# Kernel optimization log

Measured on AMD Instinct MI355X. Metric: run time of the kernel, lower is better.

The kernel has to match this reference:

```python
import jax, jax.numpy as jnp
import numpy as np

N = 100000
E = 1600000
IN_DIM = 128
HID = 128
C = 10
N_INJ = 20000
T_HET = 0.5          # self.hetero_level (set by set_adaptation_from_data)
HP_MAX = 1.0         # highpass_scale_max
INJ_LAM = 0.8        # self.inject_lambda


def setup_inputs() -> dict:
    key = jax.random.key(0)
    ks = jax.random.split(key, 16)
    glorot = lambda k, i, o: jax.random.normal(k, (i, o), jnp.float32) * (2.0 / (i + o)) ** 0.5
    return {
        "x": jax.random.normal(ks[0], (N, IN_DIM), jnp.float32),
        "edge_index": jax.random.randint(ks[1], (2, E), 0, N, jnp.int64),
        "inject_indices": jax.random.randint(ks[2], (N_INJ,), 0, N, jnp.int64),
        "initial_preds": jax.random.uniform(ks[3], (N, C), jnp.float32),
        "W1": glorot(ks[4], IN_DIM, HID), "b1": jnp.zeros((HID,), jnp.float32),
        "W2": glorot(ks[5], HID, HID),   "b2": jnp.zeros((HID,), jnp.float32),
        "Wl1": glorot(ks[6], IN_DIM, HID),
        "Wl2": glorot(ks[7], HID, HID),
        "Wm1": glorot(ks[8], HID, HID), "bm1": jnp.zeros((HID,), jnp.float32),
        "Wm2": glorot(ks[9], HID, C),   "bm2": jnp.zeros((C,), jnp.float32),
    }


def _gcn_norm(edge_index):
    # add self loops, symmetric D^{-1/2} (A+I) D^{-1/2} normalization (PyG GCNConv default)
    loops = jnp.arange(N, dtype=edge_index.dtype)
    src = jnp.concatenate([edge_index[0], loops])
    dst = jnp.concatenate([edge_index[1], loops])
    deg = jax.ops.segment_sum(jnp.ones_like(dst, jnp.float32), dst, num_segments=N)
    dinv = jnp.where(deg > 0, jax.lax.rsqrt(jnp.maximum(deg, 1.0)), 0.0)
    norm = dinv[src] * dinv[dst]  # [E+N]
    return src, dst, norm


def _gcn_conv(x, W, b, src, dst, norm):
    h = x @ W                                   # [N, H]
    msg = h[src] * norm[:, None]                # gather + scale, [E+N, H]
    return jax.ops.segment_sum(msg, dst, num_segments=N) + b


def reference(x, edge_index, inject_indices, initial_preds,
              W1, b1, W2, b2, Wl1, Wl2, Wm1, bm1, Wm2, bm2):
    src, dst, norm = _gcn_norm(edge_index)
    mix = T_HET * HP_MAX

    low1 = _gcn_conv(x, W1, b1, src, dst, norm)
    high1 = x @ Wl1 - low1
    h = jax.nn.relu(low1 + mix * high1)        # dropout: eval mode (identity)

    low2 = _gcn_conv(h, W2, b2, src, dst, norm)
    high2 = h @ Wl2 - low2
    h2 = low2 + mix * high2

    logits = jax.nn.relu(h2 @ Wm1 + bm1) @ Wm2 + bm2   # [N, C]
    # indexed injection: logits[idx] = logits[idx] + lam * preds[idx]
    logits = logits.at[inject_indices].set(
        logits[inject_indices] + INJ_LAM * initial_preds[inject_indices])
    return jax.nn.log_softmax(logits, axis=1)
```

## Files before the change

kernel.cpp:

```cpp
#include <hip/hip_runtime.h>
#include <hip/hip_bf16.h>
#include <math.h>

typedef __attribute__((ext_vector_type(8))) short short8;
typedef __attribute__((ext_vector_type(4))) float f32x4;
typedef __attribute__((ext_vector_type(2))) float f32x2;

#define INJ_LAM 0.8f
#define BSH 9
#define BWD 512

__device__ inline float bf2f(unsigned short s){
  union{unsigned u; float f;} v; v.u=((unsigned)s)<<16; return v.f;
}
__device__ inline unsigned short f2bf(float f){
  __hip_bfloat16 h=__float2bfloat16(f);
  return *reinterpret_cast<unsigned short*>(&h);
}
__device__ inline unsigned pack2(float lo, float hi){
  return ((unsigned)f2bf(hi)<<16)|(unsigned)f2bf(lo);
}

__global__ void k_prep(const float* __restrict__ W1,const float* __restrict__ Wl1,
                       const float* __restrict__ W2,const float* __restrict__ Wl2,
                       const float* __restrict__ Wm1,const float* __restrict__ Wm2,
                       const float* __restrict__ b1,const float* __restrict__ b2,
                       unsigned short* __restrict__ Wt1, unsigned short* __restrict__ Wt2,
                       unsigned short* __restrict__ Wm1t, unsigned short* __restrict__ Wm2tp,
                       float* __restrict__ bh1, float* __restrict__ bh2,
                       unsigned* __restrict__ flags32, int nf4,
                       unsigned* __restrict__ bhist8, unsigned* __restrict__ zcur8){
  int i=blockIdx.x*blockDim.x+threadIdx.x;
  if(i<256*128){
    int c=i>>7, k=i&127;
    float v1=(c<128)?W1[k*128+c]:Wl1[k*128+(c-128)];
    float v2=(c<128)?W2[k*128+c]:Wl2[k*128+(c-128)];
    Wt1[i]=f2bf(v1); Wt2[i]=f2bf(v2);
    if(c<128) Wm1t[i]=f2bf(Wm1[k*128+c]);
    if(c<16)  Wm2tp[i]=f2bf((c<10)?Wm2[k*10+c]:0.f);
    if(i<128){ bh1[i]=0.5f*b1[i]; bh2[i]=0.5f*b2[i]; }
  }
  if(i<nf4) flags32[i]=0u;
  if(i<2048){ bhist8[i]=0u; zcur8[i]=0u; }
}

__global__ void k_bhist(const int* __restrict__ dst, unsigned* __restrict__ bhist8, int E){
  __shared__ unsigned lh[256];
  int t=threadIdx.x;
  lh[t]=0u; __syncthreads();
  int base=blockIdx.x*2048;
  #pragma unroll
  for(int k=0;k<8;k++){
    int e=base+k*256+t;
    if(e<E) atomicAdd(&lh[dst[e]>>BSH],1u);
  }
  __syncthreads();
  if(lh[t]) atomicAdd(&bhist8[t*8],lh[t]);
}

__launch_bounds__(256)
__global__ void k_bscatter(const int* __restrict__ src, const int* __restrict__ dst,
                           const unsigned* __restrict__ bhist8, unsigned* __restrict__ zcur8,
                           int* __restrict__ psrc, int* __restrict__ pdst, int E, int NBK){
  __shared__ unsigned lh[256];
  __shared__ unsigned gb[256];
  __shared__ unsigned ss[256];
  int t=threadIdx.x;
  lh[t]=0u;
  unsigned v=(t<NBK)?bhist8[t*8]:0u;
  ss[t]=v; __syncthreads();
  for(int off=1;off<256;off<<=1){
    unsigned u=(t>=off)?ss[t-off]:0u; __syncthreads();
    ss[t]+=u; __syncthreads();
  }
  unsigned bb=ss[t]-v;
  int base=blockIdx.x*2048;
  unsigned lr[8]; int bk[8], sv[8], dv_[8];
  #pragma unroll
  for(int k=0;k<8;k++){
    int e=base+k*256+t;
    if(e<E){
      int d=dst[e]; int b=d>>BSH;
      bk[k]=b; dv_[k]=d; sv[k]=src[e];
      lr[k]=atomicAdd(&lh[b],1u);
    } else bk[k]=-1;
  }
  __syncthreads();
  if(lh[t]) gb[t]=bb+atomicAdd(&zcur8[t*8],lh[t]);
  __syncthreads();
  #pragma unroll
  for(int k=0;k<8;k++){
    if(bk[k]>=0){
      unsigned p=gb[bk[k]]+lr[k];
      psrc[p]=sv[k]; pdst[p]=dv_[k];
    }
  }
}

__launch_bounds__(256)
__global__ void k_bucket(const int* __restrict__ psrc, const int* __restrict__ pdst,
                         const unsigned* __restrict__ bhist8, unsigned* __restrict__ rank,
                         unsigned* __restrict__ meta, float* __restrict__ dinv,
                         int* __restrict__ csr,
                         const int* __restrict__ inj, unsigned char* __restrict__ flag,
                         int N, int NI, int NBK){
  __shared__ unsigned lc[BWD];
  __shared__ unsigned lo[BWD];
  __shared__ unsigned ss[256];
  int b=blockIdx.x, t=threadIdx.x;
  for(int i=b*256+t;i<NI;i+=gridDim.x*256) flag[inj[i]]=1;
  unsigned v=(t<NBK)?bhist8[t*8]:0u;
  ss[t]=v; lc[t]=0u; lc[t+256]=0u;
  __syncthreads();
  for(int off=1;off<256;off<<=1){
    unsigned u=(t>=off)?ss[t-off]:0u; __syncthreads();
    ss[t]+=u; __syncthreads();
  }
  unsigned e1=ss[b];
  unsigned e0=e1-bhist8[b*8];
  __syncthreads();
  int lo_node=b<<BSH;
  for(unsigned p=e0+t;p<e1;p+=256){
    int dl=pdst[p]-lo_node;
    rank[p]=atomicAdd(&lc[dl],1u);
  }
  __syncthreads();
  unsigned c0=lc[2*t], c1=lc[2*t+1], ps=c0+c1;
  ss[t]=ps; __syncthreads();
  for(int off=1;off<256;off<<=1){
    unsigned u=(t>=off)?ss[t-off]:0u; __syncthreads();
    ss[t]+=u; __syncthreads();
  }
  unsigned excl=ss[t]-ps;
  lo[2*t]=excl; lo[2*t+1]=excl+c0;
  __syncthreads();
  #pragma unroll
  for(int k=0;k<2;k++){
    int nl=t+k*256; int node=lo_node+nl;
    if(node<N){
      unsigned c=lc[nl];
      meta[node]=(e0+lo[nl])|(c<<21);
      dinv[node]=rsqrtf((float)(c+1u));
    }
  }
  for(unsigned p=e0+t;p<e1;p+=256){
    int dl=pdst[p]-lo_node;
    csr[e0+lo[dl]+rank[p]]=psrc[p];
  }
}

template<bool FP32IN>
__device__ inline void load_afrag(const void* __restrict__ Xv, size_t arow, int l4, short8* a){
  if(FP32IN){
    const float* X=(const float*)Xv + arow*128 + l4*8;
    #pragma unroll
    for(int ks=0;ks<4;ks++){
      float4 f0=*reinterpret_cast<const float4*>(X+ks*32);
      float4 f1=*reinterpret_cast<const float4*>(X+ks*32+4);
      short8 t;
      t[0]=(short)f2bf(f0.x); t[1]=(short)f2bf(f0.y); t[2]=(short)f2bf(f0.z); t[3]=(short)f2bf(f0.w);
      t[4]=(short)f2bf(f1.x); t[5]=(short)f2bf(f1.y); t[6]=(short)f2bf(f1.z); t[7]=(short)f2bf(f1.w);
      a[ks]=t;
    }
  }else{
    const unsigned short* X=(const unsigned short*)Xv + arow*128 + l4*8;
    #pragma unroll
    for(int ks=0;ks<4;ks++)
      a[ks]=*reinterpret_cast<const short8*>(X+ks*32);
  }
}

template<bool FP32IN>
__launch_bounds__(256, 4)
__global__ void k_gemm(const void* __restrict__ Xv, const unsigned short* __restrict__ Wt,
                       const float* __restrict__ dinv,
                       unsigned short* __restrict__ G, unsigned short* __restrict__ XL, int N){
  int wave=threadIdx.x>>6, lane=threadIdx.x&63;
  int l15=lane&15, l4=lane>>4;
  int blk0=blockIdx.x*128;
  if(blk0>=N) return;
  short8 wf[4][4];
  #pragma unroll
  for(int i=0;i<4;i++){
    int col=(wave*4+i)*16+l15;
    #pragma unroll
    for(int ks=0;ks<4;ks++)
      wf[i][ks]=*reinterpret_cast<const short8*>(Wt+(size_t)col*128+ks*32+l4*8);
  }
  int r0=blk0+l15; if(r0>N-1) r0=N-1;
  short8 aC[4], aN[4];
  load_afrag<FP32IN>(Xv,(size_t)r0,l4,aC);
  #pragma unroll 1
  for(int nt=0;nt<8;nt++){
    int node0=blk0+nt*16;
    if(node0>=N) break;
    if(nt<7){
      int rn=node0+16+l15; if(rn>N-1) rn=N-1;
      load_afrag<FP32IN>(Xv,(size_t)rn,l4,aN);
    }
    f32x4 acc[4];
    #pragma unroll
    for(int i=0;i<4;i++) acc[i]=(f32x4){0.f,0.f,0.f,0.f};
    #pragma unroll
    for(int i=0;i<4;i++){
      #pragma unroll
      for(int ks=0;ks<4;ks++)
        acc[i]=__builtin_amdgcn_mfma_f32_16x16x32_bf16(wf[i][ks],aC[ks],acc[i],0,0,0);
    }
    int node=node0+l15;
    if(node<N){
      if(wave<2){
        float dv=dinv[node];
        #pragma unroll
        for(int i=0;i<4;i++){
          f32x4 v=acc[i];
          uint2 p; p.x=pack2(v[0]*dv,v[1]*dv); p.y=pack2(v[2]*dv,v[3]*dv);
          *reinterpret_cast<uint2*>(G+(size_t)node*128+(wave*4+i)*16+l4*4)=p;
        }
      }else{
        #pragma unroll
        for(int i=0;i<4;i++){
          f32x4 v=acc[i];
          uint2 p; p.x=pack2(v[0]*0.5f,v[1]*0.5f); p.y=pack2(v[2]*0.5f,v[3]*0.5f);
          *reinterpret_cast<uint2*>(XL+(size_t)node*128+((wave-2)*4+i)*16+l4*4)=p;
        }
      }
    }
    #pragma unroll
    for(int ks=0;ks<4;ks++) aC[ks]=aN[ks];
  }
}

#define ADDQ(v) do{ \
  unsigned ux=(unsigned)(v).x, uy=(unsigned)(v).y, uz=(unsigned)(v).z, uw=(unsigned)(v).w; \
  accv[0]+=(f32x2){__uint_as_float(ux<<16),__uint_as_float(ux&0xffff0000u)}; \
  accv[1]+=(f32x2){__uint_as_float(uy<<16),__uint_as_float(uy&0xffff0000u)}; \
  accv[2]+=(f32x2){__uint_as_float(uz<<16),__uint_as_float(uz&0xffff0000u)}; \
  accv[3]+=(f32x2){__uint_as_float(uw<<16),__uint_as_float(uw&0xffff0000u)}; \
}while(0)

template<bool RELU>
__device__ __forceinline__ void conv_node(int node, int N,
    const unsigned short* __restrict__ G, const unsigned short* __restrict__ XL,
    const float* __restrict__ bh, const float* __restrict__ dinv,
    const int* __restrict__ csr, const unsigned* __restrict__ meta,
    unsigned short* __restrict__ ldsrow, int lane){
  if(node>=N) return;
  int g=lane>>4, li=lane&15;
  const int4* Gv=(const int4*)G;
  const int4 Z={0,0,0,0};
  f32x2 accv[4];
  #pragma unroll
  for(int i=0;i<4;i++) accv[i]=(f32x2){0.f,0.f};
  if(g==0){
    int4 v=Gv[(size_t)node*16+li];
    ADDQ(v);
  }
  unsigned mt=meta[node];
  unsigned start=mt&0x1FFFFFu, deg=mt>>21;
  unsigned j=(unsigned)g;
  int4 v0=Z,v1=Z,v2=Z,v3=Z;
  if(j<deg)    v0=Gv[(size_t)csr[start+j]*16+li];
  if(j+4<deg)  v1=Gv[(size_t)csr[start+j+4]*16+li];
  if(j+8<deg)  v2=Gv[(size_t)csr[start+j+8]*16+li];
  if(j+12<deg) v3=Gv[(size_t)csr[start+j+12]*16+li];
  j+=16;
  while(j<deg){
    int4 n0=Gv[(size_t)csr[start+j]*16+li];
    int4 n1=(j+4<deg)?Gv[(size_t)csr[start+j+4]*16+li]:Z;
    int4 n2=(j+8<deg)?Gv[(size_t)csr[start+j+8]*16+li]:Z;
    int4 n3=(j+12<deg)?Gv[(size_t)csr[start+j+12]*16+li]:Z;
    ADDQ(v0); ADDQ(v1); ADDQ(v2); ADDQ(v3);
    v0=n0; v1=n1; v2=n2; v3=n3; j+=16;
  }
  ADDQ(v0); ADDQ(v1); ADDQ(v2); ADDQ(v3);
  float acc[8];
  #pragma unroll
  for(int i=0;i<4;i++){ acc[2*i]=accv[i][0]; acc[2*i+1]=accv[i][1]; }
  #pragma unroll
  for(int i=0;i<8;i++){
    acc[i]+=__shfl_xor(acc[i],16,64);
    acc[i]+=__shfl_xor(acc[i],32,64);
  }
  if(g==0){
    float dv2=0.5f*dinv[node];
    float4 b0=*reinterpret_cast<const float4*>(bh+li*8);
    float4 b1=*reinterpret_cast<const float4*>(bh+li*8+4);
    int4 xv=((const int4*)XL)[(size_t)node*16+li];
    float xl[8];
    { unsigned _x=(unsigned)xv.x,_y=(unsigned)xv.y,_z=(unsigned)xv.z,_w=(unsigned)xv.w;
      xl[0]=bf2f((unsigned short)(_x&0xffffu)); xl[1]=bf2f((unsigned short)(_x>>16));
      xl[2]=bf2f((unsigned short)(_y&0xffffu)); xl[3]=bf2f((unsigned short)(_y>>16));
      xl[4]=bf2f((unsigned short)(_z&0xffffu)); xl[5]=bf2f((unsigned short)(_z>>16));
      xl[6]=bf2f((unsigned short)(_w&0xffffu)); xl[7]=bf2f((unsigned short)(_w>>16)); }
    float bb[8]={b0.x,b0.y,b0.z,b0.w,b1.x,b1.y,b1.z,b1.w};
    float r[8];
    #pragma unroll
    for(int i=0;i<8;i++){
      r[i]=dv2*acc[i]+bb[i]+xl[i];
      if(RELU) r[i]=fmaxf(r[i],0.f);
    }
    int4 o;
    o.x=(int)pack2(r[0],r[1]); o.y=(int)pack2(r[2],r[3]);
    o.z=(int)pack2(r[4],r[5]); o.w=(int)pack2(r[6],r[7]);
    *reinterpret_cast<int4*>(ldsrow+li*8)=o;
  }
}

__launch_bounds__(1024)
__global__ void k_convg(const unsigned short* __restrict__ G1, const unsigned short* __restrict__ XL1,
                        const float* __restrict__ bh1, const float* __restrict__ dinv,
                        const int* __restrict__ csr, const unsigned* __restrict__ meta,
                        const unsigned short* __restrict__ Wt2,
                        unsigned short* __restrict__ G2, unsigned short* __restrict__ XL2, int N){
  __shared__ __align__(16) unsigned short ht[16][136];
  int wave=threadIdx.x>>6, lane=threadIdx.x&63;
  int l15=lane&15, l4=lane>>4;
  int blk0=blockIdx.x*16;
  conv_node<true>(blk0+wave, N, G1, XL1, bh1, dinv, csr, meta, &ht[wave][0], lane);
  __syncthreads();
  short8 wfr[4], a[4];
  #pragma unroll
  for(int ks=0;ks<4;ks++){
    wfr[ks]=*reinterpret_cast<const short8*>(Wt2+(size_t)(wave*16+l15)*128+ks*32+l4*8);
    a[ks]=*reinterpret_cast<const short8*>(&ht[l15][ks*32+l4*8]);
  }
  f32x4 acc=(f32x4){0.f,0.f,0.f,0.f};
  #pragma unroll
  for(int ks=0;ks<4;ks++)
    acc=__builtin_amdgcn_mfma_f32_16x16x32_bf16(wfr[ks],a[ks],acc,0,0,0);
  int node=blk0+l15;
  if(node<N){
    if(wave<8){
      float dv=dinv[node];
      uint2 p; p.x=pack2(acc[0]*dv,acc[1]*dv); p.y=pack2(acc[2]*dv,acc[3]*dv);
      *reinterpret_cast<uint2*>(G2+(size_t)node*128+wave*16+l4*4)=p;
    }else{
      uint2 p; p.x=pack2(acc[0]*0.5f,acc[1]*0.5f); p.y=pack2(acc[2]*0.5f,acc[3]*0.5f);
      *reinterpret_cast<uint2*>(XL2+(size_t)node*128+(wave-8)*16+l4*4)=p;
    }
  }
}

__launch_bounds__(1024)
__global__ void k_convm(const unsigned short* __restrict__ G2, const unsigned short* __restrict__ XL2,
                        const float* __restrict__ bh2, const float* __restrict__ dinv,
                        const int* __restrict__ csr, const unsigned* __restrict__ meta,
                        const unsigned short* __restrict__ Wm1t, const unsigned short* __restrict__ Wm2tp,
                        const float* __restrict__ bm1, const float* __restrict__ bm2,
                        const unsigned char* __restrict__ flag, const float* __restrict__ preds,
                        float* __restrict__ out, int N){
  __shared__ __align__(16) unsigned short ht[16][136];
  __shared__ __align__(16) unsigned short zt[16][136];
  int wave=threadIdx.x>>6, lane=threadIdx.x&63;
  int l15=lane&15, l4=lane>>4;
  int blk0=blockIdx.x*16;
  conv_node<false>(blk0+wave, N, G2, XL2, bh2, dinv, csr, meta, &ht[wave][0], lane);
  __syncthreads();
  if(wave<8){
    int ct=wave;
    short8 wfr[4], a[4];
    #pragma unroll
    for(int ks=0;ks<4;ks++){
      wfr[ks]=*reinterpret_cast<const short8*>(Wm1t+(size_t)(ct*16+l15)*128+ks*32+l4*8);
      a[ks]=*reinterpret_cast<const short8*>(&ht[l15][ks*32+l4*8]);
    }
    f32x4 acc=(f32x4){0.f,0.f,0.f,0.f};
    #pragma unroll
    for(int ks=0;ks<4;ks++)
      acc=__builtin_amdgcn_mfma_f32_16x16x32_bf16(wfr[ks],a[ks],acc,0,0,0);
    float4 bm=*reinterpret_cast<const float4*>(bm1+ct*16+l4*4);
    uint2 p;
    p.x=pack2(fmaxf(acc[0]+bm.x,0.f),fmaxf(acc[1]+bm.y,0.f));
    p.y=pack2(fmaxf(acc[2]+bm.z,0.f),fmaxf(acc[3]+bm.w,0.f));
    *reinterpret_cast<uint2*>(&zt[l15][ct*16+l4*4])=p;
  }
  __syncthreads();
  if(wave==0){
    short8 a2[4], w2[4];
    #pragma unroll
    for(int ks=0;ks<4;ks++){
      a2[ks]=*reinterpret_cast<const short8*>(&zt[l15][ks*32+l4*8]);
      w2[ks]=*reinterpret_cast<const short8*>(Wm2tp+(size_t)l15*128+ks*32+l4*8);
    }
    f32x4 acc2=(f32x4){0.f,0.f,0.f,0.f};
    #pragma unroll
    for(int ks=0;ks<4;ks++)
      acc2=__builtin_amdgcn_mfma_f32_16x16x32_bf16(w2[ks],a2[ks],acc2,0,0,0);
    int node=blk0+l15;
    bool have=node<N;
    int c0=l4*4;
    float v[4];
    #pragma unroll
    for(int k=0;k<4;k++){
      int c=c0+k;
      v[k]=(c<10)?(acc2[k]+bm2[c]):-3.0e38f;
    }
    if(have && c0<10 && flag[node]){
      #pragma unroll
      for(int k=0;k<4;k++){
        int c=c0+k;
        if(c<10) v[k]+=INJ_LAM*preds[(size_t)node*10+c];
      }
    }
    float m=fmaxf(fmaxf(v[0],v[1]),fmaxf(v[2],v[3]));
    m=fmaxf(m,__shfl_xor(m,16,64));
    m=fmaxf(m,__shfl_xor(m,32,64));
    float s=0.f;
    #pragma unroll
    for(int k=0;k<4;k++){ int c=c0+k; if(c<10) s+=expf(v[k]-m); }
    s+=__shfl_xor(s,16,64);
    s+=__shfl_xor(s,32,64);
    float lse=m+logf(s);
    if(have && c0<10){
      float2 o01; o01.x=v[0]-lse; o01.y=v[1]-lse;
      *reinterpret_cast<float2*>(out+(size_t)node*10+c0)=o01;
      if(c0+2<10){
        float2 o23; o23.x=v[2]-lse; o23.y=v[3]-lse;
        *reinterpret_cast<float2*>(out+(size_t)node*10+c0+2)=o23;
      }
    }
  }
}

extern "C" void kernel_launch(void* const* d_in, const int* in_sizes, int n_in,
                              void* d_out, int out_size, void* d_ws, size_t ws_size,
                              hipStream_t stream){
  const float* x    =(const float*)d_in[0];
  const int*   ei   =(const int*)  d_in[1];
  const int*   inj  =(const int*)  d_in[2];
  const float* preds=(const float*)d_in[3];
  const float* W1 =(const float*)d_in[4];  const float* b1 =(const float*)d_in[5];
  const float* W2 =(const float*)d_in[6];  const float* b2 =(const float*)d_in[7];
  const float* Wl1=(const float*)d_in[8];  const float* Wl2=(const float*)d_in[9];
  const float* Wm1=(const float*)d_in[10]; const float* bm1=(const float*)d_in[11];
  const float* Wm2=(const float*)d_in[12]; const float* bm2=(const float*)d_in[13];
  float* out=(float*)d_out;

  const int N  = in_sizes[0]/128;
  const int E  = in_sizes[1]/2;
  const int NI = in_sizes[2];
  const int* srcp = ei;
  const int* dstp = ei+E;
  const int NBK = (N+BWD-1)>>BSH;

  char* w=(char*)d_ws;
  auto carve=[&](size_t sz)->char*{ char* p=w; w+=(sz+255)&~(size_t)255; return p; };
  unsigned short* S1 =(unsigned short*)carve((size_t)N*128*2);
  unsigned short* S2 =(unsigned short*)carve((size_t)N*128*2);
  unsigned short* S3 =(unsigned short*)carve((size_t)N*128*2);
  unsigned short* Wt1=(unsigned short*)carve(256*128*2);
  unsigned short* Wt2=(unsigned short*)carve(256*128*2);
  unsigned short* Wm1t=(unsigned short*)carve(128*128*2);
  unsigned short* Wm2tp=(unsigned short*)carve(16*128*2);
  float*    dinv  =(float*)   carve((size_t)N*4);
  unsigned* meta  =(unsigned*)carve((size_t)N*4);
  int*      csr   =(int*)     carve((size_t)E*4);
  unsigned char* flags=(unsigned char*)carve(((size_t)N+3)&~(size_t)3);
  unsigned* bhist8=(unsigned*)carve(256*8*4);
  unsigned* zcur8 =(unsigned*)carve(256*8*4);
  float* bh1=(float*)carve(128*4);
  float* bh2=(float*)carve(128*4);
  (void)ws_size; (void)n_in; (void)out_size;

  int* psrc=(int*)S3;
  int* pdst=psrc+E;
  unsigned* rank=(unsigned*)S1;

  const int T=256;
  const int EB=(E+2047)/2048;
  const int nf4=(N+3)/4;
  int gp=(32768>nf4?32768:nf4); gp=(gp+T-1)/T;
  hipLaunchKernelGGL(k_prep, dim3(gp), dim3(T), 0, stream,
                     W1,Wl1,W2,Wl2,Wm1,Wm2,b1,b2,
                     Wt1,Wt2,Wm1t,Wm2tp,bh1,bh2,
                     (unsigned*)flags, nf4, bhist8, zcur8);
  hipLaunchKernelGGL(k_bhist, dim3(EB), dim3(T), 0, stream, dstp, bhist8, E);
  hipLaunchKernelGGL(k_bscatter, dim3(EB), dim3(T), 0, stream, srcp, dstp, bhist8, zcur8,
                     psrc, pdst, E, NBK);
  hipLaunchKernelGGL(k_bucket, dim3(NBK), dim3(T), 0, stream, psrc, pdst, bhist8, rank,
                     meta, dinv, csr, inj, flags, N, NI, NBK);
  hipLaunchKernelGGL(k_gemm<true>, dim3((N+127)/128), dim3(T), 0, stream,
                     (const void*)x, Wt1, dinv, S1, S2, N);
  hipLaunchKernelGGL(k_convg, dim3((N+15)/16), dim3(1024), 0, stream,
                     S1, S2, bh1, dinv, csr, meta, Wt2, S2, S3, N);
  hipLaunchKernelGGL(k_convm, dim3((N+15)/16), dim3(1024), 0, stream,
                     S2, S3, bh2, dinv, csr, meta, Wm1t, Wm2tp, bm1, bm2,
                     flags, preds, out, N);
}
```

Measured before the change: 373.6 us.

## Process nodes in degree-sorted order in conv kernels to balance block work

Builds a per-node degree histogram during bucketing and adds a counting-sort kernel that produces a degree-ordered node permutation. Both aggregation kernels then take their nodes through this permutation, so the 16 waves sharing a block and its barrier have similar neighbour counts and wait less on the slowest wave. The cost is one extra small kernel, extra atomics, and per-node indirection that scatters the output-row and metadata accesses that were contiguous before.

```diff
diff --git a/kernel.cpp b/kernel.cpp
--- a/kernel.cpp
+++ b/kernel.cpp
@@ -29,7 +29,8 @@
                        unsigned short* __restrict__ Wm1t, unsigned short* __restrict__ Wm2tp,
                        float* __restrict__ bh1, float* __restrict__ bh2,
                        unsigned* __restrict__ flags32, int nf4,
-                       unsigned* __restrict__ bhist8, unsigned* __restrict__ zcur8){
+                       unsigned* __restrict__ bhist8, unsigned* __restrict__ zcur8,
+                       unsigned* __restrict__ dhist8, unsigned* __restrict__ dcur8){
   int i=blockIdx.x*blockDim.x+threadIdx.x;
   if(i<256*128){
     int c=i>>7, k=i&127;
@@ -42,6 +43,7 @@
   }
   if(i<nf4) flags32[i]=0u;
   if(i<2048){ bhist8[i]=0u; zcur8[i]=0u; }
+  if(i<512){ dhist8[i]=0u; dcur8[i]=0u; }
 }
 
 __global__ void k_bhist(const int* __restrict__ dst, unsigned* __restrict__ bhist8, int E){
@@ -103,14 +105,17 @@
                          unsigned* __restrict__ meta, float* __restrict__ dinv,
                          int* __restrict__ csr,
                          const int* __restrict__ inj, unsigned char* __restrict__ flag,
+                         unsigned* __restrict__ dhist8,
                          int N, int NI, int NBK){
   __shared__ unsigned lc[BWD];
   __shared__ unsigned lo[BWD];
   __shared__ unsigned ss[256];
+  __shared__ unsigned dh[64];
   int b=blockIdx.x, t=threadIdx.x;
   for(int i=b*256+t;i<NI;i+=gridDim.x*256) flag[inj[i]]=1;
   unsigned v=(t<NBK)?bhist8[t*8]:0u;
   ss[t]=v; lc[t]=0u; lc[t+256]=0u;
+  if(t<64) dh[t]=0u;
   __syncthreads();
   for(int off=1;off<256;off<<=1){
     unsigned u=(t>=off)?ss[t-off]:0u; __syncthreads();
@@ -141,12 +146,42 @@
       unsigned c=lc[nl];
       meta[node]=(e0+lo[nl])|(c<<21);
       dinv[node]=rsqrtf((float)(c+1u));
+      unsigned bin=c; if(bin>63u) bin=63u;
+      atomicAdd(&dh[bin],1u);
     }
   }
   for(unsigned p=e0+t;p<e1;p+=256){
     int dl=pdst[p]-lo_node;
     csr[e0+lo[dl]+rank[p]]=psrc[p];
   }
+  __syncthreads();
+  if(t<64 && dh[t]) atomicAdd(&dhist8[t*8],dh[t]);
+}
+
+__launch_bounds__(256)
+__global__ void k_perm(const unsigned* __restrict__ meta,
+                       const unsigned* __restrict__ dhist8, unsigned* __restrict__ dcur8,
+                       int* __restrict__ perm, int N){
+  __shared__ unsigned base[64];
+  __shared__ unsigned lh[64];
+  __shared__ unsigned gb[64];
+  int t=threadIdx.x;
+  if(t<64){
+    unsigned s=0;
+    for(int j=0;j<t;j++) s+=dhist8[j*8];
+    base[t]=s; lh[t]=0u;
+  }
+  __syncthreads();
+  int i=blockIdx.x*256+t;
+  unsigned d=0, lr=0;
+  if(i<N){
+    d=meta[i]>>21; if(d>63u) d=63u;
+    lr=atomicAdd(&lh[d],1u);
+  }
+  __syncthreads();
+  if(t<64 && lh[t]) gb[t]=atomicAdd(&dcur8[t*8],lh[t]);
+  __syncthreads();
+  if(i<N) perm[base[d]+gb[d]+lr]=i;
 }
 
 template<bool FP32IN>
@@ -311,13 +346,16 @@
 __global__ void k_convg(const unsigned short* __restrict__ G1, const unsigned short* __restrict__ XL1,
                         const float* __restrict__ bh1, const float* __restrict__ dinv,
                         const int* __restrict__ csr, const unsigned* __restrict__ meta,
+                        const int* __restrict__ perm,
                         const unsigned short* __restrict__ Wt2,
                         unsigned short* __restrict__ G2, unsigned short* __restrict__ XL2, int N){
   __shared__ __align__(16) unsigned short ht[16][136];
   int wave=threadIdx.x>>6, lane=threadIdx.x&63;
   int l15=lane&15, l4=lane>>4;
   int blk0=blockIdx.x*16;
-  conv_node<true>(blk0+wave, N, G1, XL1, bh1, dinv, csr, meta, &ht[wave][0], lane);
+  int idx=blk0+wave;
+  int node=(idx<N)?perm[idx]:N;
+  conv_node<true>(node, N, G1, XL1, bh1, dinv, csr, meta, &ht[wave][0], lane);
   __syncthreads();
   short8 wfr[4], a[4];
   #pragma unroll
@@ -329,15 +367,16 @@
   #pragma unroll
   for(int ks=0;ks<4;ks++)
     acc=__builtin_amdgcn_mfma_f32_16x16x32_bf16(wfr[ks],a[ks],acc,0,0,0);
-  int node=blk0+l15;
-  if(node<N){
+  int idx2=blk0+l15;
+  int onode=(idx2<N)?perm[idx2]:-1;
+  if(onode>=0){
     if(wave<8){
-      float dv=dinv[node];
+      float dv=dinv[onode];
       uint2 p; p.x=pack2(acc[0]*dv,acc[1]*dv); p.y=pack2(acc[2]*dv,acc[3]*dv);
-      *reinterpret_cast<uint2*>(G2+(size_t)node*128+wave*16+l4*4)=p;
+      *reinterpret_cast<uint2*>(G2+(size_t)onode*128+wave*16+l4*4)=p;
     }else{
       uint2 p; p.x=pack2(acc[0]*0.5f,acc[1]*0.5f); p.y=pack2(acc[2]*0.5f,acc[3]*0.5f);
-      *reinterpret_cast<uint2*>(XL2+(size_t)node*128+(wave-8)*16+l4*4)=p;
+      *reinterpret_cast<uint2*>(XL2+(size_t)onode*128+(wave-8)*16+l4*4)=p;
     }
   }
 }
@@ -346,6 +385,7 @@
 __global__ void k_convm(const unsigned short* __restrict__ G2, const unsigned short* __restrict__ XL2,
                         const float* __restrict__ bh2, const float* __restrict__ dinv,
                         const int* __restrict__ csr, const unsigned* __restrict__ meta,
+                        const int* __restrict__ perm,
                         const unsigned short* __restrict__ Wm1t, const unsigned short* __restrict__ Wm2tp,
                         const float* __restrict__ bm1, const float* __restrict__ bm2,
                         const unsigned char* __restrict__ flag, const float* __restrict__ preds,
@@ -355,7 +395,9 @@
   int wave=threadIdx.x>>6, lane=threadIdx.x&63;
   int l15=lane&15, l4=lane>>4;
   int blk0=blockIdx.x*16;
-  conv_node<false>(blk0+wave, N, G2, XL2, bh2, dinv, csr, meta, &ht[wave][0], lane);
+  int idx=blk0+wave;
+  int node=(idx<N)?perm[idx]:N;
+  conv_node<false>(node, N, G2, XL2, bh2, dinv, csr, meta, &ht[wave][0], lane);
   __syncthreads();
   if(wave<8){
     int ct=wave;
@@ -387,8 +429,9 @@
     #pragma unroll
     for(int ks=0;ks<4;ks++)
       acc2=__builtin_amdgcn_mfma_f32_16x16x32_bf16(w2[ks],a2[ks],acc2,0,0,0);
-    int node=blk0+l15;
-    bool have=node<N;
+    int idx2=blk0+l15;
+    int onode=(idx2<N)?perm[idx2]:-1;
+    bool have=onode>=0;
     int c0=l4*4;
     float v[4];
     #pragma unroll
@@ -396,11 +439,11 @@
       int c=c0+k;
       v[k]=(c<10)?(acc2[k]+bm2[c]):-3.0e38f;
     }
-    if(have && c0<10 && flag[node]){
+    if(have && c0<10 && flag[onode]){
       #pragma unroll
       for(int k=0;k<4;k++){
         int c=c0+k;
-        if(c<10) v[k]+=INJ_LAM*preds[(size_t)node*10+c];
+        if(c<10) v[k]+=INJ_LAM*preds[(size_t)onode*10+c];
       }
     }
     float m=fmaxf(fmaxf(v[0],v[1]),fmaxf(v[2],v[3]));
@@ -414,10 +457,10 @@
     float lse=m+logf(s);
     if(have && c0<10){
       float2 o01; o01.x=v[0]-lse; o01.y=v[1]-lse;
-      *reinterpret_cast<float2*>(out+(size_t)node*10+c0)=o01;
+      *reinterpret_cast<float2*>(out+(size_t)onode*10+c0)=o01;
       if(c0+2<10){
         float2 o23; o23.x=v[2]-lse; o23.y=v[3]-lse;
-        *reinterpret_cast<float2*>(out+(size_t)node*10+c0+2)=o23;
+        *reinterpret_cast<float2*>(out+(size_t)onode*10+c0+2)=o23;
       }
     }
   }
@@ -459,6 +502,9 @@
   unsigned char* flags=(unsigned char*)carve(((size_t)N+3)&~(size_t)3);
   unsigned* bhist8=(unsigned*)carve(256*8*4);
   unsigned* zcur8 =(unsigned*)carve(256*8*4);
+  unsigned* dhist8=(unsigned*)carve(64*8*4);
+  unsigned* dcur8 =(unsigned*)carve(64*8*4);
+  int*      perm  =(int*)carve((size_t)N*4);
   float* bh1=(float*)carve(128*4);
   float* bh2=(float*)carve(128*4);
   (void)ws_size; (void)n_in; (void)out_size;
@@ -474,17 +520,18 @@
   hipLaunchKernelGGL(k_prep, dim3(gp), dim3(T), 0, stream,
                      W1,Wl1,W2,Wl2,Wm1,Wm2,b1,b2,
                      Wt1,Wt2,Wm1t,Wm2tp,bh1,bh2,
-                     (unsigned*)flags, nf4, bhist8, zcur8);
+                     (unsigned*)flags, nf4, bhist8, zcur8, dhist8, dcur8);
   hipLaunchKernelGGL(k_bhist, dim3(EB), dim3(T), 0, stream, dstp, bhist8, E);
   hipLaunchKernelGGL(k_bscatter, dim3(EB), dim3(T), 0, stream, srcp, dstp, bhist8, zcur8,
                      psrc, pdst, E, NBK);
   hipLaunchKernelGGL(k_bucket, dim3(NBK), dim3(T), 0, stream, psrc, pdst, bhist8, rank,
-                     meta, dinv, csr, inj, flags, N, NI, NBK);
+                     meta, dinv, csr, inj, flags, dhist8, N, NI, NBK);
+  hipLaunchKernelGGL(k_perm, dim3((N+T-1)/T), dim3(T), 0, stream, meta, dhist8, dcur8, perm, N);
   hipLaunchKernelGGL(k_gemm<true>, dim3((N+127)/128), dim3(T), 0, stream,
                      (const void*)x, Wt1, dinv, S1, S2, N);
   hipLaunchKernelGGL(k_convg, dim3((N+15)/16), dim3(1024), 0, stream,
-                     S1, S2, bh1, dinv, csr, meta, Wt2, S2, S3, N);
+                     S1, S2, bh1, dinv, csr, meta, perm, Wt2, S2, S3, N);
   hipLaunchKernelGGL(k_convm, dim3((N+15)/16), dim3(1024), 0, stream,
-                     S2, S3, bh2, dinv, csr, meta, Wm1t, Wm2tp, bm1, bm2,
+                     S2, S3, bh2, dinv, csr, meta, perm, Wm1t, Wm2tp, bm1, bm2,
                      flags, preds, out, N);
 }
```

Result: slower. 402.4 us (+7.7%).
